# Kernel optimization log

Hardware: AMD Instinct MI355X
Metric: run time of the kernel (lower is better)

## Reference

```python
import jax, jax.numpy as jnp
import numpy as np

KS = 3
N = KS * KS
LN_EPS = 1e-5


def conv2d(x, w, stride=1, pad=0):
    return jax.lax.conv_general_dilated(
        x, w, (stride, stride), [(pad, pad), (pad, pad)],
        dimension_numbers=('NCHW', 'OIHW', 'NCHW'))


def layer_norm(x, g, b):
    mu = jnp.mean(x, axis=-1, keepdims=True)
    var = jnp.mean(jnp.square(x - mu), axis=-1, keepdims=True)
    return (x - mu) * jax.lax.rsqrt(var + LN_EPS) * g + b


def l2norm(x):
    n = jnp.sqrt(jnp.sum(jnp.square(x), axis=-1, keepdims=True))
    return x / jnp.maximum(n, 1e-12)


def deform_conv(x, w_p, b_p, w_d):
    # canonical DeformConv2d (kernel 3, pad 1, stride 1, no modulation)
    B, C, H, W = x.shape
    off = conv2d(x, w_p, stride=1, pad=1) + b_p[None, :, None, None]  # [B,2N,H,W]
    xp = jnp.pad(x, ((0, 0), (0, 0), (1, 1), (1, 1)))
    Hp, Wp = H + 2, W + 2
    pn = jnp.stack(jnp.meshgrid(jnp.arange(-1, 2), jnp.arange(-1, 2), indexing='ij'), 0)
    pn = pn.reshape(2, N).astype(x.dtype)  # kernel offsets, row-major (dx,dy)
    p0x = jnp.arange(1, H + 1, dtype=x.dtype)
    p0y = jnp.arange(1, W + 1, dtype=x.dtype)
    # sampling coords, [B,H,W,N]
    px = off[:, :N].transpose(0, 2, 3, 1) + p0x[None, :, None, None] + pn[0][None, None, None, :]
    py = off[:, N:].transpose(0, 2, 3, 1) + p0y[None, None, :, None] + pn[1][None, None, None, :]
    fx = jnp.floor(px)
    fy = jnp.floor(py)
    qlx = jnp.clip(fx, 0, Hp - 1)
    qly = jnp.clip(fy, 0, Wp - 1)
    qrx = jnp.clip(fx + 1, 0, Hp - 1)
    qry = jnp.clip(fy + 1, 0, Wp - 1)
    pxc = jnp.clip(px, 0, Hp - 1)
    pyc = jnp.clip(py, 0, Wp - 1)
    g_lt = (1 + (qlx - pxc)) * (1 + (qly - pyc))
    g_rb = (1 - (qrx - pxc)) * (1 - (qry - pyc))
    g_lb = (1 + (qlx - pxc)) * (1 - (qry - pyc))
    g_rt = (1 - (qrx - pxc)) * (1 + (qly - pyc))
    xf = xp.reshape(B, C, Hp * Wp)

    def gat(ix, iy):
        idx = (ix.astype(jnp.int32) * Wp + iy.astype(jnp.int32)).reshape(B, 1, -1)
        g = jnp.take_along_axis(xf, jnp.broadcast_to(idx, (B, C, idx.shape[-1])), axis=2)
        return g.reshape(B, C, H, W, N)

    xo = (g_lt[:, None] * gat(qlx, qly) + g_rb[:, None] * gat(qrx, qry)
          + g_lb[:, None] * gat(qlx, qry) + g_rt[:, None] * gat(qrx, qly))
    # [B,C,H,W,N] -> [B,C,H*ks,W*ks] (row = h*ks+kr, col = w*ks+kc)
    xo = xo.reshape(B, C, H, W, KS, KS).transpose(0, 1, 2, 4, 3, 5).reshape(B, C, H * KS, W * KS)
    return conv2d(xo, w_d, stride=KS, pad=0)


def setup_inputs() -> dict:
    key = jax.random.key(0)
    ks = jax.random.split(key, 8)
    B, C, H, W, heads = 4, 192, 64, 64, 6
    hid = 4 * C
    return {
        'x': jax.random.normal(ks[0], (B, C, H, W), dtype=jnp.float32),
        'gamma1': jnp.ones((C,), jnp.float32),
        'beta1': jnp.zeros((C,), jnp.float32),
        'gamma2': jnp.ones((C,), jnp.float32),
        'beta2': jnp.zeros((C,), jnp.float32),
        'temperature': jnp.ones((heads, 1, 1), jnp.float32),
        'w_qkv': jax.random.normal(ks[1], (3 * C, C), jnp.float32) * 0.02,
        'w_proj': jax.random.normal(ks[2], (C, C), jnp.float32) * 0.02,
        'w_p': jax.random.normal(ks[3], (2 * N, C, KS, KS), jnp.float32) * 0.01,
        'b_p': jnp.zeros((2 * N,), jnp.float32),
        'w_d': jax.random.normal(ks[4], (C, C, KS, KS), jnp.float32) * 0.02,
        'w_fc1': jax.random.normal(ks[5], (C, hid), jnp.float32) * 0.02,
        'b_fc1': jnp.zeros((hid,), jnp.float32),
        'w_fc2': jax.random.normal(ks[6], (hid, C), jnp.float32) * 0.02,
        'b_fc2': jnp.zeros((C,), jnp.float32),
    }


def reference(x, gamma1, beta1, gamma2, beta2, temperature, w_qkv, w_proj,
              w_p, b_p, w_d, w_fc1, b_fc1, w_fc2, b_fc2):
    B, C, H, W = x.shape
    heads = temperature.shape[0]
    xs = x.reshape(B, C, H * W).transpose(0, 2, 1)  # [B,HW,C]
    shortcut = xs
    xn = layer_norm(xs, gamma1, beta1).transpose(0, 2, 1).reshape(B, C, H, W)
    # SSA: deformable-conv query + channel attention over C
    q = deform_conv(xn, w_p, b_p, w_d)
    qkv = jnp.einsum('bchw,oc->bohw', xn, w_qkv)
    k_spe, v_spe = qkv[:, C:2 * C], qkv[:, 2 * C:]

    def split(t):
        return t.reshape(B, heads, C // heads, H * W)

    qh = split(q)
    kh = l2norm(split(k_spe))
    vh = l2norm(split(v_spe))
    attn = jnp.einsum('bhcn,bhdn->bhcd', qh, kh) * temperature[None]
    attn = jax.nn.softmax(attn, axis=-1)
    out = jnp.einsum('bhcd,bhdn->bhcn', attn, vh).reshape(B, C, H, W)
    out = jnp.einsum('bchw,oc->bohw', out, w_proj)
    xs2 = shortcut + out.reshape(B, C, H * W).transpose(0, 2, 1)
    h1 = layer_norm(xs2, gamma2, beta2)
    m = jax.nn.gelu(h1 @ w_fc1 + b_fc1, approximate=False) @ w_fc2 + b_fc2
    xs3 = xs2 + m
    return xs3.transpose(0, 2, 1).reshape(B, C, H, W)
```

## Files before the change

### kernel.cpp

```cpp
#include <hip/hip_runtime.h>
#include <math.h>

typedef unsigned short u16;
typedef unsigned int u32;
typedef short s16x8 __attribute__((ext_vector_type(8)));
typedef float f32x4 __attribute__((ext_vector_type(4)));

#define AS1 __attribute__((address_space(1)))
#define AS3 __attribute__((address_space(3)))

__device__ __forceinline__ float bf2f(u16 u) {
    union { u32 i; float f; } v; v.i = ((u32)u) << 16; return v.f;
}
__device__ __forceinline__ u16 f2bf(float f) {
    union { float f; u32 i; } v; v.f = f;
    u32 r = v.i + 0x7fffu + ((v.i >> 16) & 1u);
    return (u16)(r >> 16);
}
__device__ __forceinline__ void gll16(const u16* g, u16* l) {
    __builtin_amdgcn_global_load_lds((const AS1 u32*)g, (AS3 u32*)l, 16, 0, 0);
}

__global__ void prep_kernel(const float* __restrict__ wd, const float* __restrict__ wqkv,
                            const float* __restrict__ wfc1, const float* __restrict__ wfc2,
                            const float* __restrict__ wp,
                            u16* __restrict__ wdT, u16* __restrict__ wkvT,
                            u16* __restrict__ wf1T, u16* __restrict__ wf2T,
                            u16* __restrict__ wpT)
{
    int i = blockIdx.x * 256 + threadIdx.x;
    if (i < 331776) {
        int o = i / 1728, r = i % 1728;
        int p = r / 192, c = r % 192;
        wdT[i] = f2bf(wd[(o * 192 + c) * 9 + p]);
    }
    if (i < 73728) {
        int o = i / 192, c = i % 192;
        wkvT[i] = f2bf(wqkv[(192 + o) * 192 + c]);
    }
    if (i < 147456) {
        int n = i / 192, c = i % 192;
        wf1T[i] = f2bf(wfc1[c * 768 + n]);
        int n2 = i / 768, hh = i % 768;
        wf2T[i] = f2bf(wfc2[hh * 192 + n2]);
    }
    if (i < 31104) {
        int n = i / 1728, r = i % 1728;
        int p = r / 192, c = r % 192;
        wpT[i] = f2bf(wp[(n * 192 + c) * 9 + p]);
    } else if (i < 55296) {
        wpT[i] = 0;
    }
}

__global__ __launch_bounds__(256) void ln1_kernel(const float* __restrict__ x,
                                                  const float* __restrict__ g,
                                                  const float* __restrict__ be,
                                                  u16* __restrict__ xn)
{
    __shared__ float red0[256], red1[256];
    __shared__ float mu_s[64], rs_s[64];
    __shared__ u16 tile[64 * 194];
    int t = threadIdx.x, tl = t & 63, cg = t >> 6;
    int m0 = blockIdx.x * 64;
    int b = m0 >> 12, hw0 = m0 & 4095;
    const float* xb = x + (size_t)b * 786432 + hw0 + tl;
    float s = 0.f, s2 = 0.f;
    for (int cc = cg; cc < 192; cc += 4) { float v = xb[cc * 4096]; s += v; s2 += v * v; }
    red0[t] = s; red1[t] = s2;
    __syncthreads();
    if (t < 64) {
        float a = red0[t] + red0[64 + t] + red0[128 + t] + red0[192 + t];
        float q = red1[t] + red1[64 + t] + red1[128 + t] + red1[192 + t];
        float mu = a * (1.f / 192.f);
        float var = q * (1.f / 192.f) - mu * mu;
        mu_s[t] = mu; rs_s[t] = rsqrtf(var + 1e-5f);
    }
    __syncthreads();
    float mu = mu_s[tl], rs = rs_s[tl];
    for (int cc = cg; cc < 192; cc += 4) {
        float v = (xb[cc * 4096] - mu) * rs * g[cc] + be[cc];
        tile[tl * 194 + cc] = f2bf(v);
    }
    __syncthreads();
    u32* dst = (u32*)(xn + (size_t)m0 * 192);
    for (int i = t; i < 64 * 96; i += 256) {
        int r = i / 96, c2 = i % 96;
        dst[i] = *(const u32*)&tile[r * 194 + c2 * 2];
    }
}

__global__ __launch_bounds__(256) void offconv_kernel(const u16* __restrict__ xn,
                                                      const u16* __restrict__ wpT,
                                                      const float* __restrict__ bp,
                                                      float* __restrict__ off)
{
    __shared__ u16 As[64 * 200];
    __shared__ u16 Bs[32 * 200];
    int bh = blockIdx.x;
    int b = bh >> 6, h = bh & 63;
    int t = threadIdx.x;
    int lane = t & 63, wv = t >> 6;
    f32x4 acc[2];
#pragma unroll
    for (int j = 0; j < 2; j++) { acc[j][0] = 0.f; acc[j][1] = 0.f; acc[j][2] = 0.f; acc[j][3] = 0.f; }
    int r = t >> 2, cq = (t & 3) * 48;
    for (int p = 0; p < 9; p++) {
        int dh = p / 3 - 1, dw = p % 3 - 1;
        int hr = h + dh, wr = r + dw;
        bool valid = (hr >= 0) && (hr < 64) && (wr >= 0) && (wr < 64);
        const u16* src = xn + ((size_t)(b * 4096 + hr * 64 + wr)) * 192 + cq;
#pragma unroll
        for (int j = 0; j < 6; j++) {
            s16x8 v = {0, 0, 0, 0, 0, 0, 0, 0};
            if (valid) v = *(const s16x8*)(src + j * 8);
            *(s16x8*)&As[r * 200 + cq + j * 8] = v;
        }
#pragma unroll
        for (int i = 0; i < 3; i++) {
            int q = t + i * 256;
            int n = q / 24, c8 = q % 24;
            *(s16x8*)&Bs[n * 200 + c8 * 8] =
                *(const s16x8*)(wpT + n * 1728 + p * 192 + c8 * 8);
        }
        __syncthreads();
#pragma unroll
        for (int kc = 0; kc < 6; kc++) {
            s16x8 af = *(const s16x8*)&As[(wv * 16 + (lane & 15)) * 200 + kc * 32 + (lane >> 4) * 8];
            s16x8 b0 = *(const s16x8*)&Bs[(lane & 15) * 200 + kc * 32 + (lane >> 4) * 8];
            s16x8 b1 = *(const s16x8*)&Bs[(16 + (lane & 15)) * 200 + kc * 32 + (lane >> 4) * 8];
            acc[0] = __builtin_amdgcn_mfma_f32_16x16x32_bf16(af, b0, acc[0], 0, 0, 0);
            acc[1] = __builtin_amdgcn_mfma_f32_16x16x32_bf16(af, b1, acc[1], 0, 0, 0);
        }
        __syncthreads();
    }
    int col = lane & 15;
    int wbase = wv * 16 + (lane >> 4) * 4;
#pragma unroll
    for (int j = 0; j < 2; j++) {
        int n = j * 16 + col;
        if (n < 18) {
            float bb = bp[n];
#pragma unroll
            for (int rr = 0; rr < 4; rr++) {
                int w = wbase + rr;
                off[((size_t)(b * 4096 + h * 64 + w)) * 18 + n] = acc[j][rr] + bb;
            }
        }
    }
}

__global__ __launch_bounds__(512) void gemm_deform(const u16* __restrict__ xn,
                                                   const float* __restrict__ off,
                                                   const u16* __restrict__ wdT,
                                                   u16* __restrict__ qt)
{
    __shared__ u16 Bs[24 * 96 * 8];
    __shared__ u16 As[64 * 200];
    __shared__ u32 tbl[64 * 9 * 4];
    int t = threadIdx.x, lane = t & 63, wv = t >> 6;
    int m0 = blockIdx.x * 64;
    int n0 = blockIdx.y * 96;
    int b = m0 >> 12;
    for (int i = t; i < 576; i += 512) {
        int mi = i / 9, p = i % 9;
        int m = m0 + mi, hw = m & 4095;
        int h = hw >> 6, w = hw & 63;
        float ox = off[(size_t)m * 18 + p];
        float oy = off[(size_t)m * 18 + 9 + p];
        float px = ox + (float)(h + 1) + (float)(p / 3 - 1);
        float py = oy + (float)(w + 1) + (float)(p % 3 - 1);
        float fx = floorf(px), fy = floorf(py);
        float qlx = fminf(fmaxf(fx, 0.f), 65.f);
        float qly = fminf(fmaxf(fy, 0.f), 65.f);
        float qrx = fminf(fmaxf(fx + 1.f, 0.f), 65.f);
        float qry = fminf(fmaxf(fy + 1.f, 0.f), 65.f);
        float pxc = fminf(fmaxf(px, 0.f), 65.f);
        float pyc = fminf(fmaxf(py, 0.f), 65.f);
        float gxl = 1.f + (qlx - pxc), gxr = 1.f - (qrx - pxc);
        float gyl = 1.f + (qly - pyc), gyr = 1.f - (qry - pyc);
        int xl = (int)qlx, xr = (int)qrx, yl = (int)qly, yr = (int)qry;
        int cx[4] = {xl, xr, xl, xr};
        int cy[4] = {yl, yr, yr, yl};
        float cw[4] = {gxl * gyl, gxr * gyr, gxl * gyr, gxr * gyl};
#pragma unroll
        for (int k = 0; k < 4; k++) {
            bool ok = (cx[k] >= 1) && (cx[k] <= 64) && (cy[k] >= 1) && (cy[k] <= 64);
            u32 tok = (u32)(b * 4096 + (cx[k] - 1) * 64 + (cy[k] - 1));
            tbl[(mi * 9 + p) * 4 + k] = ok ? ((tok << 16) | (u32)f2bf(cw[k])) : 0u;
        }
    }
    int gboff[5];
    int nch = 0;
    for (int c = wv; c < 36; c += 8) {
        int u = c * 64 + lane;
        int k8 = u / 96, n = u - k8 * 96;
        gboff[nch++] = (n0 + n) * 1728 + k8 * 8;
    }
    __syncthreads();
    f32x4 acc[3];
#pragma unroll
    for (int j = 0; j < 3; j++) { acc[j][0] = 0.f; acc[j][1] = 0.f; acc[j][2] = 0.f; acc[j][3] = 0.f; }
    int wm = wv & 3, wn = wv >> 2;
    for (int p = 0; p < 9; p++) {
        {
            int c = wv;
            for (int i = 0; i < nch; i++, c += 8)
                gll16(wdT + gboff[i] + p * 192, Bs + c * 512);
        }
        for (int i = t; i < 1536; i += 512) {
            int mi = i / 24, ch = (i % 24) * 8;
            const u32* te = &tbl[(mi * 9 + p) * 4];
            float v[8] = {0.f, 0.f, 0.f, 0.f, 0.f, 0.f, 0.f, 0.f};
#pragma unroll
            for (int k = 0; k < 4; k++) {
                u32 e = te[k];
                float wt = bf2f((u16)(e & 0xffffu));
                s16x8 cv = *(const s16x8*)(xn + (size_t)(e >> 16) * 192 + ch);
#pragma unroll
                for (int j = 0; j < 8; j++) v[j] += wt * bf2f((u16)cv[j]);
            }
            s16x8 ov;
#pragma unroll
            for (int j = 0; j < 8; j++) ov[j] = (short)f2bf(v[j]);
            *(s16x8*)&As[mi * 200 + ch] = ov;
        }
        asm volatile("s_waitcnt vmcnt(0)" ::: "memory");
        __syncthreads();
#pragma unroll
        for (int kk = 0; kk < 6; kk++) {
            s16x8 af = *(const s16x8*)&As[(wm * 16 + (lane & 15)) * 200 + kk * 32 + (lane >> 4) * 8];
#pragma unroll
            for (int j = 0; j < 3; j++) {
                s16x8 bfr = *(const s16x8*)&Bs[(((kk * 4 + (lane >> 4)) * 96) + wn * 48 + j * 16 + (lane & 15)) * 8];
                acc[j] = __builtin_amdgcn_mfma_f32_16x16x32_bf16(af, bfr, acc[j], 0, 0, 0);
            }
        }
        __syncthreads();
    }
    int mmb = m0 + wm * 16 + ((lane >> 4) << 2);
#pragma unroll
    for (int j = 0; j < 3; j++) {
        int nn = n0 + wn * 48 + j * 16 + (lane & 15);
#pragma unroll
        for (int r = 0; r < 4; r++)
            qt[(size_t)(mmb + r) * 192 + nn] = f2bf(acc[j][r]);
    }
}

template<int BM, int BN, int WM, int WN, int EP>
__global__ __launch_bounds__((BM / WM) * (BN / WN) * 64)
void gemm_bt(const u16* __restrict__ A, int lda,
             const u16* __restrict__ B, int ldb, int bstride,
             void* __restrict__ out, int ldc,
             const float* __restrict__ ex1, int K)
{
    constexpr int BK = 32;
    constexpr int WAVES_M = BM / WM, WAVES_N = BN / WN, NW = WAVES_M * WAVES_N;
    constexpr int TM = WM / 16, TN = WN / 16;
    constexpr int NLA = BM / 16, NLB = BN / 16;
    __shared__ u16 As[BM * BK];
    __shared__ u16 Bs[BN * BK];
    int tid = threadIdx.x;
    int lane = tid & 63, wv = tid >> 6;
    int wm = wv % WAVES_M, wn = wv / WAVES_M;
    int m0 = blockIdx.x * BM, n0 = blockIdx.y * BN;
    const u16* Bp = B + (size_t)(m0 >> 12) * bstride;
    f32x4 acc[TM][TN];
#pragma unroll
    for (int i = 0; i < TM; i++)
#pragma unroll
        for (int j = 0; j < TN; j++) {
            acc[i][j][0] = 0.f; acc[i][j][1] = 0.f; acc[i][j][2] = 0.f; acc[i][j][3] = 0.f;
        }
    int arow_l = lane >> 2;
    int acol_l = (lane & 3) * 8;
    for (int k0 = 0; k0 < K; k0 += BK) {
#pragma unroll 1
        for (int j = wv; j < NLA + NLB; j += NW) {
            if (j < NLA) {
                int row = j * 16 + arow_l;
                gll16(A + (size_t)(m0 + row) * lda + k0 + acol_l, As + j * 512);
            } else {
                int row = (j - NLA) * 16 + arow_l;
                gll16(Bp + (size_t)(n0 + row) * ldb + k0 + acol_l, Bs + (j - NLA) * 512);
            }
        }
        asm volatile("s_waitcnt vmcnt(0)" ::: "memory");
        __syncthreads();
        s16x8 af[TM], bfr[TN];
#pragma unroll
        for (int i = 0; i < TM; i++)
            af[i] = *(const s16x8*)&As[(wm * WM + i * 16 + (lane & 15)) * BK + (lane >> 4) * 8];
#pragma unroll
        for (int j = 0; j < TN; j++)
            bfr[j] = *(const s16x8*)&Bs[(wn * WN + j * 16 + (lane & 15)) * BK + (lane >> 4) * 8];
#pragma unroll
        for (int i = 0; i < TM; i++)
#pragma unroll
            for (int j = 0; j < TN; j++)
                acc[i][j] = __builtin_amdgcn_mfma_f32_16x16x32_bf16(af[i], bfr[j], acc[i][j], 0, 0, 0);
        __syncthreads();
    }
    int col = lane & 15;
#pragma unroll
    for (int i = 0; i < TM; i++)
#pragma unroll
        for (int j = 0; j < TN; j++) {
            int mm = m0 + wm * WM + i * 16 + (lane >> 4) * 4;
            int nn = n0 + wn * WN + j * 16 + col;
            if (EP == 0) {
                u16* o = (u16*)out;
#pragma unroll
                for (int r = 0; r < 4; r++) o[(size_t)(mm + r) * ldc + nn] = f2bf(acc[i][j][r]);
            } else if (EP == 1) {
                float* o = (float*)out;
                const float* xr = ex1 + (size_t)(mm >> 12) * 786432 + (size_t)nn * 4096 + (mm & 4095);
#pragma unroll
                for (int r = 0; r < 4; r++) o[(size_t)(mm + r) * ldc + nn] = acc[i][j][r] + xr[r];
            } else if (EP == 2) {
                u16* o = (u16*)out;
                float bb = ex1[nn];
#pragma unroll
                for (int r = 0; r < 4; r++) {
                    float v = acc[i][j][r] + bb;
                    o[(size_t)(mm + r) * ldc + nn] = f2bf(0.5f * v * (1.f + erff(v * 0.70710678118654752f)));
                }
            } else {
                float* o = (float*)out;
                float bb = ex1[nn];
#pragma unroll
                for (int r = 0; r < 4; r++) o[(size_t)(mm + r) * ldc + nn] = acc[i][j][r] + bb;
            }
        }
}

__global__ __launch_bounds__(384) void norm_kernel(const u16* __restrict__ kv,
                                                   float* __restrict__ norm2)
{
    int b = blockIdx.y, ch = blockIdx.x;
    int t = threadIdx.x;
    const u16* base = kv + ((size_t)(b * 4096 + ch * 128)) * 384 + t;
    float s = 0.f;
    for (int r = 0; r < 128; r++) { float v = bf2f(base[(size_t)r * 384]); s += v * v; }
    atomicAdd(&norm2[b * 384 + t], s);
}

__global__ __launch_bounds__(64) void attnp_kernel(const u16* __restrict__ qt,
                                                   const u16* __restrict__ kvt,
                                                   float* __restrict__ raw)
{
    __shared__ float qT[32 * 69];
    __shared__ float kT[32 * 69];
    int ch = blockIdx.x, h = blockIdx.y, b = blockIdx.z;
    int t = threadIdx.x;
    size_t base = (size_t)(b * 4096 + ch * 64);
    for (int e = t; e < 2048; e += 64) {
        int r = e >> 5, c = e & 31;
        qT[c * 69 + r] = bf2f(qt[(base + r) * 192 + h * 32 + c]);
        kT[c * 69 + r] = bf2f(kvt[(base + r) * 384 + h * 32 + c]);
    }
    __syncthreads();
    int tc = t >> 3, td = t & 7;
    int c0 = tc * 4, d0 = td * 4;
    float acc[4][4] = {};
    for (int r = 0; r < 64; r++) {
        float qv[4], kv4[4];
#pragma unroll
        for (int u = 0; u < 4; u++) { qv[u] = qT[(c0 + u) * 69 + r]; kv4[u] = kT[(d0 + u) * 69 + r]; }
#pragma unroll
        for (int u = 0; u < 4; u++)
#pragma unroll
            for (int v = 0; v < 4; v++) acc[u][v] += qv[u] * kv4[v];
    }
    float* dst = raw + ((size_t)(b * 6 + h)) * 1024;
#pragma unroll
    for (int u = 0; u < 4; u++)
#pragma unroll
        for (int v = 0; v < 4; v++)
            atomicAdd(&dst[(c0 + u) * 32 + d0 + v], acc[u][v]);
}

__global__ __launch_bounds__(1024) void softmax_kernel(const float* __restrict__ raw,
                                                       const float* __restrict__ norm2,
                                                       const float* __restrict__ temp,
                                                       float* __restrict__ att2)
{
    int h = blockIdx.x, b = blockIdx.y;
    int t = threadIdx.x;
    int c = t >> 5, d = t & 31;
    __shared__ float invk[32], invv[32];
    if (t < 32)       invk[t] = 1.f / fmaxf(sqrtf(norm2[b * 384 + h * 32 + t]), 1e-12f);
    else if (t < 64)  invv[t - 32] = 1.f / fmaxf(sqrtf(norm2[b * 384 + 192 + h * 32 + (t - 32)]), 1e-12f);
    __syncthreads();
    float T = temp[h];
    float v = raw[((size_t)(b * 6 + h) * 32 + c) * 32 + d] * invk[d] * T;
    float mx = v;
    for (int s = 16; s > 0; s >>= 1) mx = fmaxf(mx, __shfl_xor(mx, s, 32));
    float e = expf(v - mx);
    float sm = e;
    for (int s = 16; s > 0; s >>= 1) sm += __shfl_xor(sm, s, 32);
    att2[((size_t)(b * 6 + h) * 32 + c) * 32 + d] = (e / sm) * invv[d];
}

__global__ __launch_bounds__(192) void mb_kernel(const float* __restrict__ wproj,
                                                 const float* __restrict__ att2,
                                                 u16* __restrict__ Mb)
{
    int o2 = blockIdx.x, b = blockIdx.y, t = threadIdx.x;
    int h = t >> 5, d = t & 31;
    float s = 0.f;
#pragma unroll
    for (int c = 0; c < 32; c++)
        s += wproj[o2 * 192 + h * 32 + c] * att2[((size_t)(b * 6 + h) * 32 + c) * 32 + d];
    Mb[((size_t)b * 192 + o2) * 192 + t] = f2bf(s);
}

__global__ __launch_bounds__(256) void ln2_kernel(const float* __restrict__ xs2,
                                                  const float* __restrict__ g,
                                                  const float* __restrict__ be,
                                                  u16* __restrict__ h1)
{
    int t = threadIdx.x;
    int wv = t >> 6, l = t & 63;
    size_t m = (size_t)blockIdx.x * 4 + wv;
    const float* row = xs2 + m * 192;
    float v0 = row[l], v1 = row[l + 64], v2 = row[l + 128];
    float s = v0 + v1 + v2, s2 = v0 * v0 + v1 * v1 + v2 * v2;
    for (int sh = 32; sh > 0; sh >>= 1) { s += __shfl_xor(s, sh); s2 += __shfl_xor(s2, sh); }
    float mu = s * (1.f / 192.f);
    float var = s2 * (1.f / 192.f) - mu * mu;
    float rs = rsqrtf(var + 1e-5f);
    u16* o = h1 + m * 192;
    o[l]       = f2bf((v0 - mu) * rs * g[l]       + be[l]);
    o[l + 64]  = f2bf((v1 - mu) * rs * g[l + 64]  + be[l + 64]);
    o[l + 128] = f2bf((v2 - mu) * rs * g[l + 128] + be[l + 128]);
}

__global__ __launch_bounds__(256) void final_kernel(const float* __restrict__ xs2,
                                                    const float* __restrict__ m2,
                                                    float* __restrict__ out)
{
    __shared__ float tile[192 * 65];
    int blk = blockIdx.x;
    int b = blk >> 6, hw0 = (blk & 63) * 64;
    int t = threadIdx.x;
    size_t mbase = ((size_t)b * 4096 + hw0) * 192;
    for (int i = t; i < 64 * 192; i += 256) {
        int r = i / 192, c = i % 192;
        tile[c * 65 + r] = xs2[mbase + i] + m2[mbase + i];
    }
    __syncthreads();
    for (int i = t; i < 64 * 192; i += 256) {
        int c = i / 64, r = i % 64;
        out[(size_t)b * 786432 + (size_t)c * 4096 + hw0 + r] = tile[c * 65 + r];
    }
}

extern "C" void kernel_launch(void* const* d_in, const int* in_sizes, int n_in,
                              void* d_out, int out_size, void* d_ws, size_t ws_size,
                              hipStream_t stream)
{
    const float* x      = (const float*)d_in[0];
    const float* gamma1 = (const float*)d_in[1];
    const float* beta1  = (const float*)d_in[2];
    const float* gamma2 = (const float*)d_in[3];
    const float* beta2  = (const float*)d_in[4];
    const float* temp   = (const float*)d_in[5];
    const float* w_qkv  = (const float*)d_in[6];
    const float* w_proj = (const float*)d_in[7];
    const float* w_p    = (const float*)d_in[8];
    const float* b_p    = (const float*)d_in[9];
    const float* w_d    = (const float*)d_in[10];
    const float* w_fc1  = (const float*)d_in[11];
    const float* b_fc1  = (const float*)d_in[12];
    const float* w_fc2  = (const float*)d_in[13];
    const float* b_fc2  = (const float*)d_in[14];
    float* out = (float*)d_out;
    char* ws = (char*)d_ws;

    u16*   xn    = (u16*)(ws + 0);
    float* off   = (float*)(ws + 6291456);
    u16*   adef  = (u16*)(ws + 7471104);
    u16*   wpT   = adef;
    u16*   m1    = adef;
    float* m2    = (float*)(ws + 7471104 + 25165824);
    u16*   qt    = (u16*)(ws + 64094208);
    u16*   kvt   = (u16*)(ws + 70385664);
    float* norm2 = (float*)(ws + 82968576);
    float* araw  = (float*)(ws + 82974720);
    float* att2  = (float*)(ws + 83073024);
    u16*   Mb    = (u16*)(ws + 83171328);
    float* xs2   = (float*)(ws + 83318784);
    u16*   h1    = xn;
    u16*   wdT   = (u16*)(ws + 95901696);
    u16*   wkvT  = (u16*)(ws + 96565248);
    u16*   wf1T  = (u16*)(ws + 96712704);
    u16*   wf2T  = (u16*)(ws + 97007616);

    hipMemsetAsync(norm2, 0, 6144 + 98304, stream);
    prep_kernel<<<1296, 256, 0, stream>>>(w_d, w_qkv, w_fc1, w_fc2, w_p, wdT, wkvT, wf1T, wf2T, wpT);
    ln1_kernel<<<256, 256, 0, stream>>>(x, gamma1, beta1, xn);
    offconv_kernel<<<256, 256, 0, stream>>>(xn, wpT, b_p, off);
    gemm_deform<<<dim3(256, 2), 512, 0, stream>>>(xn, off, wdT, qt);
    gemm_bt<128, 128, 64, 64, 0><<<dim3(128, 3), 256, 0, stream>>>(xn, 192, wkvT, 192, 0, kvt, 384, nullptr, 192);
    norm_kernel<<<dim3(32, 4), 384, 0, stream>>>(kvt, norm2);
    attnp_kernel<<<dim3(64, 6, 4), 64, 0, stream>>>(qt, kvt, araw);
    softmax_kernel<<<dim3(6, 4), 1024, 0, stream>>>(araw, norm2, temp, att2);
    mb_kernel<<<dim3(192, 4), 192, 0, stream>>>(w_proj, att2, Mb);
    gemm_bt<32, 192, 32, 96, 1><<<dim3(512, 1), 128, 0, stream>>>(kvt + 192, 384, Mb, 192, 192 * 192, xs2, 192, x, 192);
    ln2_kernel<<<4096, 256, 0, stream>>>(xs2, gamma2, beta2, h1);
    gemm_bt<128, 128, 64, 64, 2><<<dim3(128, 6), 256, 0, stream>>>(h1, 192, wf1T, 192, 0, m1, 768, b_fc1, 192);
    gemm_bt<32, 192, 32, 96, 3><<<dim3(512, 1), 128, 0, stream>>>(m1, 768, wf2T, 768, 0, m2, 192, b_fc2, 768);
    final_kernel<<<256, 256, 0, stream>>>(xs2, m2, out);
}
```

Before: 296.1 us.

## Restructure deformable GEMM: full-N tile, register A operand, double-buffered weight chunks

Each gemm_deform block now covers all 192 output channels, so bilinear sampling is no longer repeated across two N-blocks. The weights are pre-swizzled into contiguous 64-K chunks and streamed into double-buffered LDS. Each wave builds its A fragments for the next chunk directly in registers, overlapping the xn gathers with the current MFMAs and removing the A staging buffer in LDS. The costs are half as many blocks (256 instead of 512, with 256 threads), 12 accumulators per wave, and higher register pressure.

```diff
diff --git a/kernel.cpp b/kernel.cpp
--- a/kernel.cpp
+++ b/kernel.cpp
@@ -24,15 +24,19 @@
 __global__ void prep_kernel(const float* __restrict__ wd, const float* __restrict__ wqkv,
                             const float* __restrict__ wfc1, const float* __restrict__ wfc2,
                             const float* __restrict__ wp,
-                            u16* __restrict__ wdT, u16* __restrict__ wkvT,
+                            u16* __restrict__ wdS, u16* __restrict__ wkvT,
                             u16* __restrict__ wf1T, u16* __restrict__ wf2T,
                             u16* __restrict__ wpT)
 {
     int i = blockIdx.x * 256 + threadIdx.x;
     if (i < 331776) {
-        int o = i / 1728, r = i % 1728;
-        int p = r / 192, c = r % 192;
-        wdT[i] = f2bf(wd[(o * 192 + c) * 9 + p]);
+        int e = i & 7;
+        int u = (i >> 3) % 1536;
+        int chunk = i / 12288;
+        int k8 = u / 192, n = u % 192;
+        int kg = chunk * 64 + k8 * 8 + e;
+        int p = kg / 192, c = kg % 192;
+        wdS[i] = f2bf(wd[(n * 192 + c) * 9 + p]);
     }
     if (i < 73728) {
         int o = i / 192, c = i % 192;
@@ -150,20 +154,18 @@
     }
 }
 
-__global__ __launch_bounds__(512) void gemm_deform(const u16* __restrict__ xn,
+__global__ __launch_bounds__(256) void gemm_deform(const u16* __restrict__ xn,
                                                    const float* __restrict__ off,
-                                                   const u16* __restrict__ wdT,
+                                                   const u16* __restrict__ wdS,
                                                    u16* __restrict__ qt)
 {
-    __shared__ u16 Bs[24 * 96 * 8];
-    __shared__ u16 As[64 * 200];
+    __shared__ u16 Bs[2][12288];
     __shared__ u32 tbl[64 * 9 * 4];
     int t = threadIdx.x, lane = t & 63, wv = t >> 6;
     int m0 = blockIdx.x * 64;
-    int n0 = blockIdx.y * 96;
     int b = m0 >> 12;
-    for (int i = t; i < 576; i += 512) {
-        int mi = i / 9, p = i % 9;
+    for (int j = t; j < 576; j += 256) {
+        int mi = j / 9, p = j % 9;
         int m = m0 + mi, hw = m & 4095;
         int h = hw >> 6, w = hw & 63;
         float ox = off[(size_t)m * 18 + p];
@@ -190,58 +192,95 @@
             tbl[(mi * 9 + p) * 4 + k] = ok ? ((tok << 16) | (u32)f2bf(cw[k])) : 0u;
         }
     }
-    int gboff[5];
-    int nch = 0;
-    for (int c = wv; c < 36; c += 8) {
-        int u = c * 64 + lane;
-        int k8 = u / 96, n = u - k8 * 96;
-        gboff[nch++] = (n0 + n) * 1728 + k8 * 8;
-    }
-    __syncthreads();
-    f32x4 acc[3];
-#pragma unroll
-    for (int j = 0; j < 3; j++) { acc[j][0] = 0.f; acc[j][1] = 0.f; acc[j][2] = 0.f; acc[j][3] = 0.f; }
-    int wm = wv & 3, wn = wv >> 2;
-    for (int p = 0; p < 9; p++) {
-        {
-            int c = wv;
-            for (int i = 0; i < nch; i++, c += 8)
-                gll16(wdT + gboff[i] + p * 192, Bs + c * 512);
-        }
-        for (int i = t; i < 1536; i += 512) {
-            int mi = i / 24, ch = (i % 24) * 8;
-            const u32* te = &tbl[(mi * 9 + p) * 4];
-            float v[8] = {0.f, 0.f, 0.f, 0.f, 0.f, 0.f, 0.f, 0.f};
-#pragma unroll
-            for (int k = 0; k < 4; k++) {
-                u32 e = te[k];
-                float wt = bf2f((u16)(e & 0xffffu));
-                s16x8 cv = *(const s16x8*)(xn + (size_t)(e >> 16) * 192 + ch);
-#pragma unroll
-                for (int j = 0; j < 8; j++) v[j] += wt * bf2f((u16)cv[j]);
-            }
+    __syncthreads();
+    int mi = wv * 16 + (lane & 15);
+    int kq = (lane >> 4) * 8;
+    f32x4 acc[12];
+#pragma unroll
+    for (int j = 0; j < 12; j++) { acc[j][0] = 0.f; acc[j][1] = 0.f; acc[j][2] = 0.f; acc[j][3] = 0.f; }
+    s16x8 aCur[2];
+#pragma unroll
+    for (int ii = 0; ii < 6; ii++) {
+        int cs = wv + ii * 4;
+        gll16(wdS + (size_t)(cs * 64 + lane) * 8, &Bs[0][cs * 512]);
+    }
+    {
+        const u32* te = &tbl[(mi * 9 + 0) * 4];
+        u32 e0 = te[0], e1 = te[1], e2 = te[2], e3 = te[3];
+        float w0 = bf2f((u16)e0), w1 = bf2f((u16)e1), w2 = bf2f((u16)e2), w3 = bf2f((u16)e3);
+#pragma unroll
+        for (int f = 0; f < 2; f++) {
+            int ch = kq + f * 32;
+            s16x8 c0 = *(const s16x8*)(xn + (size_t)(e0 >> 16) * 192 + ch);
+            s16x8 c1 = *(const s16x8*)(xn + (size_t)(e1 >> 16) * 192 + ch);
+            s16x8 c2 = *(const s16x8*)(xn + (size_t)(e2 >> 16) * 192 + ch);
+            s16x8 c3 = *(const s16x8*)(xn + (size_t)(e3 >> 16) * 192 + ch);
             s16x8 ov;
 #pragma unroll
-            for (int j = 0; j < 8; j++) ov[j] = (short)f2bf(v[j]);
-            *(s16x8*)&As[mi * 200 + ch] = ov;
-        }
+            for (int j = 0; j < 8; j++) {
+                float v = w0 * bf2f((u16)c0[j]) + w1 * bf2f((u16)c1[j])
+                        + w2 * bf2f((u16)c2[j]) + w3 * bf2f((u16)c3[j]);
+                ov[j] = (short)f2bf(v);
+            }
+            aCur[f] = ov;
+        }
+    }
+#pragma unroll 1
+    for (int i = 0; i < 27; i++) {
         asm volatile("s_waitcnt vmcnt(0)" ::: "memory");
         __syncthreads();
-#pragma unroll
-        for (int kk = 0; kk < 6; kk++) {
-            s16x8 af = *(const s16x8*)&As[(wm * 16 + (lane & 15)) * 200 + kk * 32 + (lane >> 4) * 8];
-#pragma unroll
-            for (int j = 0; j < 3; j++) {
-                s16x8 bfr = *(const s16x8*)&Bs[(((kk * 4 + (lane >> 4)) * 96) + wn * 48 + j * 16 + (lane & 15)) * 8];
+        const u16* cur = &Bs[i & 1][0];
+        u16* nxt = &Bs[(i + 1) & 1][0];
+        u32 e0 = 0, e1 = 0, e2 = 0, e3 = 0;
+        s16x8 ct[8];
+        if (i < 26) {
+            size_t gbase = (size_t)(i + 1) * 12288;
+#pragma unroll
+            for (int ii = 0; ii < 6; ii++) {
+                int cs = wv + ii * 4;
+                gll16(wdS + gbase + (size_t)(cs * 64 + lane) * 8, nxt + cs * 512);
+            }
+            int p1 = (i + 1) / 3;
+            int ch0 = ((i + 1) % 3) * 64 + kq;
+            const u32* te = &tbl[(mi * 9 + p1) * 4];
+            e0 = te[0]; e1 = te[1]; e2 = te[2]; e3 = te[3];
+#pragma unroll
+            for (int f = 0; f < 2; f++) {
+                int ch = ch0 + f * 32;
+                ct[f * 4 + 0] = *(const s16x8*)(xn + (size_t)(e0 >> 16) * 192 + ch);
+                ct[f * 4 + 1] = *(const s16x8*)(xn + (size_t)(e1 >> 16) * 192 + ch);
+                ct[f * 4 + 2] = *(const s16x8*)(xn + (size_t)(e2 >> 16) * 192 + ch);
+                ct[f * 4 + 3] = *(const s16x8*)(xn + (size_t)(e3 >> 16) * 192 + ch);
+            }
+        }
+#pragma unroll
+        for (int f = 0; f < 2; f++) {
+            s16x8 af = aCur[f];
+#pragma unroll
+            for (int j = 0; j < 12; j++) {
+                s16x8 bfr = *(const s16x8*)&cur[(((f * 4 + (lane >> 4)) * 192) + j * 16 + (lane & 15)) * 8];
                 acc[j] = __builtin_amdgcn_mfma_f32_16x16x32_bf16(af, bfr, acc[j], 0, 0, 0);
             }
         }
-        __syncthreads();
-    }
-    int mmb = m0 + wm * 16 + ((lane >> 4) << 2);
-#pragma unroll
-    for (int j = 0; j < 3; j++) {
-        int nn = n0 + wn * 48 + j * 16 + (lane & 15);
+        if (i < 26) {
+            float w0 = bf2f((u16)e0), w1 = bf2f((u16)e1), w2 = bf2f((u16)e2), w3 = bf2f((u16)e3);
+#pragma unroll
+            for (int f = 0; f < 2; f++) {
+                s16x8 ov;
+#pragma unroll
+                for (int j = 0; j < 8; j++) {
+                    float v = w0 * bf2f((u16)ct[f * 4 + 0][j]) + w1 * bf2f((u16)ct[f * 4 + 1][j])
+                            + w2 * bf2f((u16)ct[f * 4 + 2][j]) + w3 * bf2f((u16)ct[f * 4 + 3][j]);
+                    ov[j] = (short)f2bf(v);
+                }
+                aCur[f] = ov;
+            }
+        }
+    }
+    int mmb = m0 + wv * 16 + ((lane >> 4) << 2);
+#pragma unroll
+    for (int j = 0; j < 12; j++) {
+        int nn = j * 16 + (lane & 15);
 #pragma unroll
         for (int r = 0; r < 4; r++)
             qt[(size_t)(mmb + r) * 192 + nn] = f2bf(acc[j][r]);
@@ -493,16 +532,16 @@
     u16*   Mb    = (u16*)(ws + 83171328);
     float* xs2   = (float*)(ws + 83318784);
     u16*   h1    = xn;
-    u16*   wdT   = (u16*)(ws + 95901696);
+    u16*   wdS   = (u16*)(ws + 95901696);
     u16*   wkvT  = (u16*)(ws + 96565248);
     u16*   wf1T  = (u16*)(ws + 96712704);
     u16*   wf2T  = (u16*)(ws + 97007616);
 
     hipMemsetAsync(norm2, 0, 6144 + 98304, stream);
-    prep_kernel<<<1296, 256, 0, stream>>>(w_d, w_qkv, w_fc1, w_fc2, w_p, wdT, wkvT, wf1T, wf2T, wpT);
+    prep_kernel<<<1296, 256, 0, stream>>>(w_d, w_qkv, w_fc1, w_fc2, w_p, wdS, wkvT, wf1T, wf2T, wpT);
     ln1_kernel<<<256, 256, 0, stream>>>(x, gamma1, beta1, xn);
     offconv_kernel<<<256, 256, 0, stream>>>(xn, wpT, b_p, off);
-    gemm_deform<<<dim3(256, 2), 512, 0, stream>>>(xn, off, wdT, qt);
+    gemm_deform<<<256, 256, 0, stream>>>(xn, off, wdS, qt);
     gemm_bt<128, 128, 64, 64, 0><<<dim3(128, 3), 256, 0, stream>>>(xn, 192, wkvT, 192, 0, kvt, 384, nullptr, 192);
     norm_kernel<<<dim3(32, 4), 384, 0, stream>>>(kvt, norm2);
     attnp_kernel<<<dim3(64, 6, 4), 64, 0, stream>>>(qt, kvt, araw);
```

Result: slower. 305.0 us (+3.0%).
